# Performance work log

Measured on AMD Instinct MI355X. Metric: run time of the kernel, lower is better.

Reference implementation:

```python
import jax, jax.numpy as jnp
import numpy as np

D_MODEL = 2048
NUM_HEADS = 16
HEAD_DIM = D_MODEL // NUM_HEADS


def setup_inputs() -> dict:
    key = jax.random.key(0)
    ks = jax.random.split(key, 11)
    B, S = 2, 2048
    s = 1.0 / np.sqrt(D_MODEL)
    return {
        "query": jax.random.normal(ks[0], (B, S, D_MODEL), jnp.float32),
        "key_in": jax.random.normal(ks[1], (B, S, D_MODEL), jnp.float32),
        "value": jax.random.normal(ks[2], (B, S, D_MODEL), jnp.float32),
        "Wq": jax.random.normal(ks[3], (D_MODEL, D_MODEL), jnp.float32) * s,
        "bq": jnp.zeros((D_MODEL,), jnp.float32),
        "Wk": jax.random.normal(ks[4], (D_MODEL, D_MODEL), jnp.float32) * s,
        "bk": jnp.zeros((D_MODEL,), jnp.float32),
        "Wv": jax.random.normal(ks[5], (D_MODEL, D_MODEL), jnp.float32) * s,
        "bv": jnp.zeros((D_MODEL,), jnp.float32),
        "Wo": jax.random.normal(ks[6], (D_MODEL, D_MODEL), jnp.float32) * s,
        "bo": jnp.zeros((D_MODEL,), jnp.float32),
    }


def reference(query, key_in, value, Wq, bq, Wk, bk, Wv, bv, Wo, bo):
    B, S, _ = query.shape
    # projections (torch Linear: x @ W.T + b)
    q = query @ Wq.T + bq
    k = key_in @ Wk.T + bk
    v = value @ Wv.T + bv
    # [B, H, S, Dh]
    q = q.reshape(B, S, NUM_HEADS, HEAD_DIM).transpose(0, 2, 1, 3)
    k = k.reshape(B, -1, NUM_HEADS, HEAD_DIM).transpose(0, 2, 1, 3)
    v = v.reshape(B, -1, NUM_HEADS, HEAD_DIM).transpose(0, 2, 1, 3)
    scores = jnp.einsum("bhqd,bhkd->bhqk", q, k) / np.sqrt(HEAD_DIM).astype(np.float32)
    attn = jax.nn.softmax(scores, axis=-1)
    out = jnp.einsum("bhqk,bhkd->bhqd", attn, v)
    out = out.transpose(0, 2, 1, 3).reshape(B, S, D_MODEL)
    return out @ Wo.T + bo
```

## Files before the change

kernel.cpp:

```cpp
#include <hip/hip_runtime.h>
#include <hip/hip_bf16.h>
#include <stdint.h>

typedef __hip_bfloat16 bf16;
typedef __attribute__((ext_vector_type(8))) short bf16x8;
typedef __attribute__((ext_vector_type(4))) float f32x4;
typedef __attribute__((ext_vector_type(4))) short s16x4;

constexpr int D_MODEL   = 2048;
constexpr int NUM_HEADS = 16;
constexpr int HEAD_DIM  = 128;
constexpr int BATCH     = 2;
constexpr int SEQ       = 2048;

__device__ __forceinline__ void gload_lds16(const bf16* g, bf16* l) {
    __builtin_amdgcn_global_load_lds(
        (const __attribute__((address_space(1))) void*)g,
        (__attribute__((address_space(3))) void*)l, 16, 0, 0);
}

struct CvtArgs { const float* src[7]; bf16* dst[7]; int n8[7]; };

__global__ __launch_bounds__(256)
void cvt_multi(CvtArgs a)
{
    const int t = blockIdx.y;
    const float* __restrict__ s = a.src[t];
    bf16* __restrict__ d = a.dst[t];
    const int n8 = a.n8[t];
    for (int i = blockIdx.x * 256 + threadIdx.x; i < n8; i += gridDim.x * 256) {
        f32x4 x = *(const f32x4*)(s + (size_t)i * 8);
        f32x4 y = *(const f32x4*)(s + (size_t)i * 8 + 4);
        bf16 t8[8] = { __float2bfloat16(x[0]), __float2bfloat16(x[1]),
                       __float2bfloat16(x[2]), __float2bfloat16(x[3]),
                       __float2bfloat16(y[0]), __float2bfloat16(y[1]),
                       __float2bfloat16(y[2]), __float2bfloat16(y[3]) };
        *(bf16x8*)(d + (size_t)i * 8) = *(const bf16x8*)t8;
    }
}

template <typename TC, bool TRANS_PERM>
__device__ __forceinline__
void gemm_body(const bf16* __restrict__ A, const bf16* __restrict__ W,
               const float* __restrict__ bias, TC* __restrict__ C,
               int M, int N, int K)
{
    constexpr int BM = 128, BN = 128, BK = 32;
    __shared__ bf16 sA[BM][BK];
    __shared__ bf16 sB[BN][BK];

    const int tid  = threadIdx.x;
    const int wave = tid >> 6, lane = tid & 63;
    const int quad = lane >> 4, l16 = lane & 15;
    const int wr = wave >> 1, wc = wave & 1;
    const int m0 = blockIdx.y * BM, n0 = blockIdx.x * BN;
    bf16* sAf = &sA[0][0];
    bf16* sBf = &sB[0][0];

    f32x4 acc[4][4];
#pragma unroll
    for (int i = 0; i < 4; i++)
#pragma unroll
        for (int j = 0; j < 4; j++) acc[i][j] = (f32x4){0.f, 0.f, 0.f, 0.f};

    for (int k0 = 0; k0 < K; k0 += BK) {
        __syncthreads();
#pragma unroll
        for (int s = 0; s < 2; s++) {
            int c = s * 256 + wave * 64 + lane;
            int row = c >> 2, col = (c & 3) * 8;
            gload_lds16(&A[(size_t)(m0 + row) * K + k0 + col], sAf + (size_t)c * 8);
            gload_lds16(&W[(size_t)(n0 + row) * K + k0 + col], sBf + (size_t)c * 8);
        }
        __syncthreads();

        bf16x8 af[4], bfr[4];
#pragma unroll
        for (int i = 0; i < 4; i++) af[i]  = *(const bf16x8*)&sA[wr * 64 + i * 16 + l16][quad * 8];
#pragma unroll
        for (int j = 0; j < 4; j++) bfr[j] = *(const bf16x8*)&sB[wc * 64 + j * 16 + l16][quad * 8];
#pragma unroll
        for (int i = 0; i < 4; i++)
#pragma unroll
            for (int j = 0; j < 4; j++)
                acc[i][j] = __builtin_amdgcn_mfma_f32_16x16x32_bf16(af[i], bfr[j], acc[i][j], 0, 0, 0);
    }

#pragma unroll
    for (int j = 0; j < 4; j++) {
        int col = n0 + wc * 64 + j * 16 + l16;
        float bv = bias[col];
#pragma unroll
        for (int i = 0; i < 4; i++) {
            if constexpr (TRANS_PERM) {
                int row0 = m0 + wr * 64 + i * 16 + quad * 4;
                int g    = row0 & 63;
                int tau  = g >> 4, qh = (g >> 2) & 3;
                int pp   = (tau >> 1) * 32 + qh * 8 + (tau & 1) * 4;
                int sp   = ((row0 & 2047) & ~63) | pp;
                size_t idx = (size_t)(row0 >> 11) * ((size_t)D_MODEL * SEQ)
                           + (size_t)col * SEQ + sp;
                bf16 t4[4];
#pragma unroll
                for (int r = 0; r < 4; r++) t4[r] = __float2bfloat16(acc[i][j][r] + bv);
                *(s16x4*)&C[idx] = *(const s16x4*)t4;
            } else {
#pragma unroll
                for (int r = 0; r < 4; r++) {
                    int row = m0 + wr * 64 + i * 16 + quad * 4 + r;
                    if constexpr (sizeof(TC) == 2)
                        C[(size_t)row * N + col] = (TC)__float2bfloat16(acc[i][j][r] + bv);
                    else
                        C[(size_t)row * N + col] = (TC)(acc[i][j][r] + bv);
                }
            }
        }
    }
}

template <typename TC, bool TRANS_PERM>
__global__ __launch_bounds__(256, 2)
void gemm_bf16(const bf16* __restrict__ A, const bf16* __restrict__ W,
               const float* __restrict__ bias, TC* __restrict__ C,
               int M, int N, int K)
{
    gemm_body<TC, TRANS_PERM>(A, W, bias, C, M, N, K);
}

struct QkArgs { const bf16* A[2]; const bf16* W[2]; const float* bias[2]; bf16* C[2]; };

__global__ __launch_bounds__(256, 2)
void gemm_qk(QkArgs ga, int M, int N, int K)
{
    const int z = blockIdx.z;
    gemm_body<bf16, false>(ga.A[z], ga.W[z], ga.bias[z], ga.C[z], M, N, K);
}

__global__ __launch_bounds__(256)
void flash_attn_kernel(const bf16* __restrict__ Qp, const bf16* __restrict__ Kp,
                       const bf16* __restrict__ Vt, bf16* __restrict__ Op)
{
    constexpr int BQ = 128, BKV = 64, DH = 128;
    constexpr int LDK = DH + 8;
    constexpr int LDV = BKV + 8;
    __shared__ bf16 sK[BKV][LDK];
    __shared__ bf16 sVt[DH][LDV];

    const int tid  = threadIdx.x;
    const int wave = tid >> 6, lane = tid & 63;
    const int quad = lane >> 4, l16 = lane & 15;
    const int q0 = blockIdx.x * BQ;
    const int h  = blockIdx.y;
    const int b  = blockIdx.z;

    const size_t base  = (size_t)b * SEQ * D_MODEL + (size_t)h * HEAD_DIM;
    const size_t basev = ((size_t)b * NUM_HEADS + h) * (size_t)HEAD_DIM * SEQ;

    bf16x8 bq[2][4];
#pragma unroll
    for (int nt = 0; nt < 2; nt++)
#pragma unroll
        for (int kk = 0; kk < 4; kk++)
            bq[nt][kk] = *(const bf16x8*)&Qp[base +
                (size_t)(q0 + wave * 32 + nt * 16 + l16) * D_MODEL + kk * 32 + quad * 8];

    f32x4 oacc[2][8];
#pragma unroll
    for (int nt = 0; nt < 2; nt++)
#pragma unroll
        for (int mt = 0; mt < 8; mt++) oacc[nt][mt] = (f32x4){0.f, 0.f, 0.f, 0.f};

    float lsum[2] = {0.f, 0.f};

    const float SCL2E = 0.08838834764831845f * 1.4426950408889634f;

    for (int t = 0; t < SEQ / BKV; ++t) {
        __syncthreads();
#pragma unroll
        for (int s = 0; s < 4; s++) {
            int c = tid + s * 256;
            int row = c >> 4, col = (c & 15) * 8;
            *(bf16x8*)&sK[row][col] =
                *(const bf16x8*)&Kp[base + (size_t)(t * BKV + row) * D_MODEL + col];
        }
#pragma unroll
        for (int s = 0; s < 4; s++) {
            int c = tid + s * 256;
            int dh = c >> 3, kc = (c & 7) * 8;
            *(bf16x8*)&sVt[dh][kc] =
                *(const bf16x8*)&Vt[basev + (size_t)dh * SEQ + t * BKV + kc];
        }
        __syncthreads();

        f32x4 sacc[2][4];
#pragma unroll
        for (int nt = 0; nt < 2; nt++)
#pragma unroll
            for (int kt = 0; kt < 4; kt++) sacc[nt][kt] = (f32x4){0.f, 0.f, 0.f, 0.f};
#pragma unroll
        for (int kk = 0; kk < 4; kk++) {
            bf16x8 ak[4];
#pragma unroll
            for (int kt = 0; kt < 4; kt++)
                ak[kt] = *(const bf16x8*)&sK[kt * 16 + l16][kk * 32 + quad * 8];
#pragma unroll
            for (int nt = 0; nt < 2; nt++)
#pragma unroll
                for (int kt = 0; kt < 4; kt++)
                    sacc[nt][kt] = __builtin_amdgcn_mfma_f32_16x16x32_bf16(ak[kt], bq[nt][kk], sacc[nt][kt], 0, 0, 0);
        }

        bf16x8 pb[2][2];
#pragma unroll
        for (int nt = 0; nt < 2; nt++) {
            bf16 tmp[16];
#pragma unroll
            for (int kt = 0; kt < 4; kt++) {
#pragma unroll
                for (int r = 0; r < 4; r++) {
                    float p = exp2f(fminf(sacc[nt][kt][r] * SCL2E, 60.f));
                    lsum[nt] += p;
                    tmp[(kt >> 1) * 8 + (kt & 1) * 4 + r] = __float2bfloat16(p);
                }
            }
            pb[nt][0] = *(const bf16x8*)&tmp[0];
            pb[nt][1] = *(const bf16x8*)&tmp[8];
        }

#pragma unroll
        for (int c = 0; c < 2; c++) {
#pragma unroll
            for (int mt = 0; mt < 8; mt++) {
                bf16x8 av = *(const bf16x8*)&sVt[mt * 16 + l16][c * 32 + quad * 8];
#pragma unroll
                for (int nt = 0; nt < 2; nt++)
                    oacc[nt][mt] = __builtin_amdgcn_mfma_f32_16x16x32_bf16(av, pb[nt][c], oacc[nt][mt], 0, 0, 0);
            }
        }
    }

#pragma unroll
    for (int nt = 0; nt < 2; nt++) {
        float v = lsum[nt];
        v += __shfl_xor(v, 16);
        v += __shfl_xor(v, 32);
        lsum[nt] = v;
    }

#pragma unroll
    for (int nt = 0; nt < 2; nt++) {
        float inv = 1.f / lsum[nt];
        int row = q0 + wave * 32 + nt * 16 + l16;
#pragma unroll
        for (int mt = 0; mt < 8; mt++) {
            bf16 t4[4];
#pragma unroll
            for (int r = 0; r < 4; r++) t4[r] = __float2bfloat16(oacc[nt][mt][r] * inv);
            *(s16x4*)&Op[base + (size_t)row * D_MODEL + mt * 16 + quad * 4] = *(const s16x4*)t4;
        }
    }
}

extern "C" void kernel_launch(void* const* d_in, const int* in_sizes, int n_in,
                              void* d_out, int out_size, void* d_ws, size_t ws_size,
                              hipStream_t stream)
{
    const float* query  = (const float*)d_in[0];
    const float* key_in = (const float*)d_in[1];
    const float* value  = (const float*)d_in[2];
    const float* Wq = (const float*)d_in[3];
    const float* bq = (const float*)d_in[4];
    const float* Wk = (const float*)d_in[5];
    const float* bk = (const float*)d_in[6];
    const float* Wv = (const float*)d_in[7];
    const float* bv = (const float*)d_in[8];
    const float* Wo = (const float*)d_in[9];
    const float* bo = (const float*)d_in[10];
    float* out = (float*)d_out;

    const int tokens = BATCH * SEQ;
    const size_t nAct = (size_t)tokens * D_MODEL;
    const size_t nW   = (size_t)D_MODEL * D_MODEL;

    bf16* p = (bf16*)d_ws;
    bf16* qb  = p; p += nAct;
    bf16* kb  = p; p += nAct;
    bf16* vb  = p; p += nAct;
    bf16* wqb = p; p += nW;
    bf16* wkb = p; p += nW;
    bf16* wvb = p; p += nW;
    bf16* wob = p; p += nW;
    bf16* qp  = p; p += nAct;
    bf16* kp  = p; p += nAct;
    bf16* vpT = qb;
    bf16* ap  = kb;

    CvtArgs ca;
    ca.src[0] = query;  ca.dst[0] = qb;  ca.n8[0] = (int)(nAct / 8);
    ca.src[1] = key_in; ca.dst[1] = kb;  ca.n8[1] = (int)(nAct / 8);
    ca.src[2] = value;  ca.dst[2] = vb;  ca.n8[2] = (int)(nAct / 8);
    ca.src[3] = Wq;     ca.dst[3] = wqb; ca.n8[3] = (int)(nW / 8);
    ca.src[4] = Wk;     ca.dst[4] = wkb; ca.n8[4] = (int)(nW / 8);
    ca.src[5] = Wv;     ca.dst[5] = wvb; ca.n8[5] = (int)(nW / 8);
    ca.src[6] = Wo;     ca.dst[6] = wob; ca.n8[6] = (int)(nW / 8);
    cvt_multi<<<dim3(512, 7), 256, 0, stream>>>(ca);

    QkArgs qa;
    qa.A[0] = qb; qa.W[0] = wqb; qa.bias[0] = bq; qa.C[0] = qp;
    qa.A[1] = kb; qa.W[1] = wkb; qa.bias[1] = bk; qa.C[1] = kp;
    dim3 gqk(D_MODEL / 128, tokens / 128, 2);
    gemm_qk<<<gqk, 256, 0, stream>>>(qa, tokens, D_MODEL, D_MODEL);

    dim3 gg(D_MODEL / 128, tokens / 128);
    gemm_bf16<bf16, true><<<gg, 256, 0, stream>>>(vb, wvb, bv, vpT, tokens, D_MODEL, D_MODEL);

    dim3 ga(SEQ / 128, NUM_HEADS, BATCH);
    flash_attn_kernel<<<ga, 256, 0, stream>>>(qp, kp, vpT, ap);

    gemm_bf16<float, false><<<gg, 256, 0, stream>>>(ap, wob, bo, out, tokens, D_MODEL, D_MODEL);
}
```

Measured before the change: 528.5 us.

## Double-buffer flash-attention K/V tiles with async LDS loads and fuse QKV GEMM

The flash-attention kernel now stages K and V^T tiles into two LDS buffers using direct global-to-LDS loads. An XOR swizzle replaces the old row padding to avoid bank conflicts. The next tile is prefetched while the current one is computed, so the loop needs one barrier per iteration instead of two, hiding global-load latency behind MFMA work. Separately, when the workspace is large enough, the Q, K and V projections run as one 3-slice GEMM launch with a dedicated V^T output buffer, which removes a launch and improves GPU fill, at the cost of extra workspace.

```diff
diff --git a/kernel.cpp b/kernel.cpp
--- a/kernel.cpp
+++ b/kernel.cpp
@@ -127,6 +127,16 @@
     gemm_body<TC, TRANS_PERM>(A, W, bias, C, M, N, K);
 }
 
+struct QkvArgs { const bf16* A[3]; const bf16* W[3]; const float* bias[3]; bf16* C[3]; };
+
+__global__ __launch_bounds__(256, 2)
+void gemm_qkv(QkvArgs ga, int M, int N, int K)
+{
+    const int z = blockIdx.z;
+    if (z == 2) gemm_body<bf16, true >(ga.A[2], ga.W[2], ga.bias[2], ga.C[2], M, N, K);
+    else        gemm_body<bf16, false>(ga.A[z], ga.W[z], ga.bias[z], ga.C[z], M, N, K);
+}
+
 struct QkArgs { const bf16* A[2]; const bf16* W[2]; const float* bias[2]; bf16* C[2]; };
 
 __global__ __launch_bounds__(256, 2)
@@ -141,10 +151,8 @@
                        const bf16* __restrict__ Vt, bf16* __restrict__ Op)
 {
     constexpr int BQ = 128, BKV = 64, DH = 128;
-    constexpr int LDK = DH + 8;
-    constexpr int LDV = BKV + 8;
-    __shared__ bf16 sK[BKV][LDK];
-    __shared__ bf16 sVt[DH][LDV];
+    __shared__ bf16 sK[2][BKV * DH];
+    __shared__ bf16 sV[2][DH * BKV];
 
     const int tid  = threadIdx.x;
     const int wave = tid >> 6, lane = tid & 63;
@@ -155,6 +163,29 @@
 
     const size_t base  = (size_t)b * SEQ * D_MODEL + (size_t)h * HEAD_DIM;
     const size_t basev = ((size_t)b * NUM_HEADS + h) * (size_t)HEAD_DIM * SEQ;
+    const bf16* Kb = Kp + base;
+    const bf16* Vb = Vt + basev;
+
+    auto stage = [&](int t, int bi) {
+        const bf16* Kt = Kb + (size_t)t * BKV * D_MODEL;
+        const bf16* Vtile = Vb + (size_t)t * BKV;
+        bf16* sKb = sK[bi];
+        bf16* sVb = sV[bi];
+#pragma unroll
+        for (int s = 0; s < 4; s++) {
+            int c = s * 256 + wave * 64 + lane;
+            int row = c >> 4, gs = c & 15;
+            int g = gs ^ (row & 15);
+            gload_lds16(Kt + (size_t)row * D_MODEL + g * 8, sKb + (size_t)c * 8);
+        }
+#pragma unroll
+        for (int s = 0; s < 4; s++) {
+            int c = s * 256 + wave * 64 + lane;
+            int dh = c >> 3, gs = c & 7;
+            int g = gs ^ (dh & 7);
+            gload_lds16(Vtile + (size_t)dh * SEQ + g * 8, sVb + (size_t)c * 8);
+        }
+    };
 
     bf16x8 bq[2][4];
 #pragma unroll
@@ -173,24 +204,16 @@
     float lsum[2] = {0.f, 0.f};
 
     const float SCL2E = 0.08838834764831845f * 1.4426950408889634f;
-
-    for (int t = 0; t < SEQ / BKV; ++t) {
+    constexpr int NT = SEQ / BKV;
+
+    stage(0, 0);
+
+    for (int t = 0; t < NT; ++t) {
         __syncthreads();
-#pragma unroll
-        for (int s = 0; s < 4; s++) {
-            int c = tid + s * 256;
-            int row = c >> 4, col = (c & 15) * 8;
-            *(bf16x8*)&sK[row][col] =
-                *(const bf16x8*)&Kp[base + (size_t)(t * BKV + row) * D_MODEL + col];
-        }
-#pragma unroll
-        for (int s = 0; s < 4; s++) {
-            int c = tid + s * 256;
-            int dh = c >> 3, kc = (c & 7) * 8;
-            *(bf16x8*)&sVt[dh][kc] =
-                *(const bf16x8*)&Vt[basev + (size_t)dh * SEQ + t * BKV + kc];
-        }
-        __syncthreads();
+        if (t + 1 < NT) stage(t + 1, (t + 1) & 1);
+
+        const bf16* sKc = sK[t & 1];
+        const bf16* sVc = sV[t & 1];
 
         f32x4 sacc[2][4];
 #pragma unroll
@@ -201,8 +224,11 @@
         for (int kk = 0; kk < 4; kk++) {
             bf16x8 ak[4];
 #pragma unroll
-            for (int kt = 0; kt < 4; kt++)
-                ak[kt] = *(const bf16x8*)&sK[kt * 16 + l16][kk * 32 + quad * 8];
+            for (int kt = 0; kt < 4; kt++) {
+                int row = kt * 16 + l16;
+                int g   = (kk * 4 + quad) ^ l16;
+                ak[kt] = *(const bf16x8*)&sKc[(size_t)row * DH + g * 8];
+            }
 #pragma unroll
             for (int nt = 0; nt < 2; nt++)
 #pragma unroll
@@ -231,7 +257,9 @@
         for (int c = 0; c < 2; c++) {
 #pragma unroll
             for (int mt = 0; mt < 8; mt++) {
-                bf16x8 av = *(const bf16x8*)&sVt[mt * 16 + l16][c * 32 + quad * 8];
+                int row = mt * 16 + l16;
+                int g   = (c * 4 + quad) ^ (l16 & 7);
+                bf16x8 av = *(const bf16x8*)&sVc[(size_t)row * BKV + g * 8];
 #pragma unroll
                 for (int nt = 0; nt < 2; nt++)
                     oacc[nt][mt] = __builtin_amdgcn_mfma_f32_16x16x32_bf16(av, pb[nt][c], oacc[nt][mt], 0, 0, 0);
@@ -282,6 +310,8 @@
     const size_t nAct = (size_t)tokens * D_MODEL;
     const size_t nW   = (size_t)D_MODEL * D_MODEL;
 
+    const bool fused_qkv = ws_size >= (6 * nAct + 4 * nW) * sizeof(bf16);
+
     bf16* p = (bf16*)d_ws;
     bf16* qb  = p; p += nAct;
     bf16* kb  = p; p += nAct;
@@ -292,8 +322,10 @@
     bf16* wob = p; p += nW;
     bf16* qp  = p; p += nAct;
     bf16* kp  = p; p += nAct;
-    bf16* vpT = qb;
-    bf16* ap  = kb;
+    bf16* vpT;
+    if (fused_qkv) { vpT = p; p += nAct; }
+    else           { vpT = qb; }
+    bf16* ap = fused_qkv ? qb : kb;
 
     CvtArgs ca;
     ca.src[0] = query;  ca.dst[0] = qb;  ca.n8[0] = (int)(nAct / 8);
@@ -305,17 +337,26 @@
     ca.src[6] = Wo;     ca.dst[6] = wob; ca.n8[6] = (int)(nW / 8);
     cvt_multi<<<dim3(512, 7), 256, 0, stream>>>(ca);
 
-    QkArgs qa;
-    qa.A[0] = qb; qa.W[0] = wqb; qa.bias[0] = bq; qa.C[0] = qp;
-    qa.A[1] = kb; qa.W[1] = wkb; qa.bias[1] = bk; qa.C[1] = kp;
-    dim3 gqk(D_MODEL / 128, tokens / 128, 2);
-    gemm_qk<<<gqk, 256, 0, stream>>>(qa, tokens, D_MODEL, D_MODEL);
-
-    dim3 gg(D_MODEL / 128, tokens / 128);
-    gemm_bf16<bf16, true><<<gg, 256, 0, stream>>>(vb, wvb, bv, vpT, tokens, D_MODEL, D_MODEL);
+    if (fused_qkv) {
+        QkvArgs qa;
+        qa.A[0] = qb; qa.W[0] = wqb; qa.bias[0] = bq; qa.C[0] = qp;
+        qa.A[1] = kb; qa.W[1] = wkb; qa.bias[1] = bk; qa.C[1] = kp;
+        qa.A[2] = vb; qa.W[2] = wvb; qa.bias[2] = bv; qa.C[2] = vpT;
+        dim3 g3(D_MODEL / 128, tokens / 128, 3);
+        gemm_qkv<<<g3, 256, 0, stream>>>(qa, tokens, D_MODEL, D_MODEL);
+    } else {
+        QkArgs qa;
+        qa.A[0] = qb; qa.W[0] = wqb; qa.bias[0] = bq; qa.C[0] = qp;
+        qa.A[1] = kb; qa.W[1] = wkb; qa.bias[1] = bk; qa.C[1] = kp;
+        dim3 g2(D_MODEL / 128, tokens / 128, 2);
+        gemm_qk<<<g2, 256, 0, stream>>>(qa, tokens, D_MODEL, D_MODEL);
+        dim3 gg(D_MODEL / 128, tokens / 128);
+        gemm_bf16<bf16, true><<<gg, 256, 0, stream>>>(vb, wvb, bv, vpT, tokens, D_MODEL, D_MODEL);
+    }
 
     dim3 ga(SEQ / 128, NUM_HEADS, BATCH);
     flash_attn_kernel<<<ga, 256, 0, stream>>>(qp, kp, vpT, ap);
 
+    dim3 gg(D_MODEL / 128, tokens / 128);
     gemm_bf16<float, false><<<gg, 256, 0, stream>>>(ap, wob, bo, out, tokens, D_MODEL, D_MODEL);
 }
```

Result: faster. 475.7 us (-10.0%).
